# Optimization experiments

Measured on AMD Instinct MI355X. Metric: run time of the kernel, lower is better.

Reference implementation:

```python
import jax, jax.numpy as jnp
import numpy as np

LABEL_SIZE = 64
START = LABEL_SIZE - 2
STOP = LABEL_SIZE - 1
NEG = -10000.0


def setup_inputs() -> dict:
    key = jax.random.key(0)
    k1, k2 = jax.random.split(key)
    B, T, L = 512, 512, LABEL_SIZE
    emissions = jax.random.normal(k1, (B, T, L), dtype=jnp.float32)
    # xavier-uniform-ish init, then mask row START (nothing transitions INTO start
    # ... actually transitions[next, prev]: row START = transitions into START)
    bound = float(np.sqrt(6.0 / (L + L)))
    trans = jax.random.uniform(k2, (L, L), dtype=jnp.float32, minval=-bound, maxval=bound)
    trans = trans.at[START, :].set(NEG)   # never transition to START
    trans = trans.at[:, STOP].set(NEG)    # never transition from STOP
    return {"input": emissions, "transitions": trans}


def reference(input, transitions):
    # input: [B, T, L] emission scores; transitions[next_tag, prev_tag]: [L, L]
    B, T, L = input.shape
    init = jnp.full((B, L), NEG, dtype=input.dtype).at[:, START].set(0.0)

    def step(forward_var, emit_t):
        # forward_var: [B, L] (over prev tag); emit_t: [B, L] (over next tag)
        # scores[b, next, prev] = forward_var[b, prev] + transitions[next, prev]
        nv = jax.nn.logsumexp(forward_var[:, None, :] + transitions[None, :, :], axis=-1)
        return nv + emit_t, None

    forward_var, _ = jax.lax.scan(step, init, jnp.swapaxes(input, 0, 1))  # scan over T
    terminal = forward_var + transitions[STOP][None, :]
    return jax.nn.logsumexp(terminal, axis=-1)  # [B] log partition function
```

## Files before the change

### kernel.cpp

```cpp
#include <hip/hip_runtime.h>

#define NTAG 64
#define TLEN 512
#define START_TAG 62
#define STOP_TAG 63
#define NB 16

typedef __attribute__((ext_vector_type(4))) float    f32x4;
typedef __attribute__((ext_vector_type(8))) short    s16x8;
typedef __attribute__((ext_vector_type(2))) unsigned u32x2;
typedef __attribute__((ext_vector_type(4))) unsigned u32x4;

#if __has_builtin(__builtin_amdgcn_exp2f)
#define EXP2(x) __builtin_amdgcn_exp2f(x)
#else
#define EXP2(x) exp2f(x)
#endif

__device__ __forceinline__ unsigned cvtpk_bf16(float lo, float hi) {
    unsigned r;
    asm("v_cvt_pk_bf16_f32 %0, %1, %2" : "=v"(r) : "v"(lo), "v"(hi));
    return r;
}

__device__ __forceinline__ f32x4 mfma32(s16x8 a, s16x8 b, f32x4 c) {
    return __builtin_amdgcn_mfma_f32_16x16x32_bf16(a, b, c, 0, 0, 0);
}

__global__ __launch_bounds__(128) void crf_fwd_bwd(
    const float* __restrict__ emis,
    const float* __restrict__ trans,
    float* __restrict__ out)
{
    const int tile = blockIdx.x;
    const int tid  = threadIdx.x;
    const int lane = tid & 63;
    const int w    = tid >> 6;
    const int c    = lane & 15;
    const int g    = lane >> 4;
    const int b0   = tile * NB;

    const float L2E = 1.4426950408889634f;
    const float LN2 = 0.6931471805599453f;

    __shared__ float fy[64][17];
    __shared__ int   offb_sh[16];

    s16x8 Af[4][2];
    #pragma unroll
    for (int m = 0; m < 4; ++m) {
        #pragma unroll
        for (int kt = 0; kt < 2; ++kt) {
            float ev[8];
            #pragma unroll
            for (int jj = 0; jj < 8; ++jj) {
                const int r = 16 * m + c;
                const int k = 32 * kt + 16 * (jj >> 2) + 4 * g + (jj & 3);
                const float tv = (w == 0) ? trans[r * NTAG + k]
                                          : trans[k * NTAG + r];
                ev[jj] = EXP2(tv * L2E);
            }
            u32x4 p;
            p[0] = cvtpk_bf16(ev[0], ev[1]);
            p[1] = cvtpk_bf16(ev[2], ev[3]);
            p[2] = cvtpk_bf16(ev[4], ev[5]);
            p[3] = cvtpk_bf16(ev[6], ev[7]);
            Af[m][kt] = __builtin_bit_cast(s16x8, p);
        }
    }

    const float* ebase = emis + (size_t)(b0 + c) * (TLEN * NTAG) + 4 * g;

    f32x4 wq[8][4];
    f32x4 peA[4], peB[4];
    u32x2 Bf[4];
    f32x4 ym[4];
    int   off = 0;
    int   erA = 0, erB = 0;

    #define PREF_F(slot, t) do {                                       \
        const float* _p = ebase + (t) * NTAG;                          \
        wq[slot][0] = *(const f32x4*)(_p +  0);                        \
        wq[slot][1] = *(const f32x4*)(_p + 16);                        \
        wq[slot][2] = *(const f32x4*)(_p + 32);                        \
        wq[slot][3] = *(const f32x4*)(_p + 48);                        \
    } while (0)
    #define PREF_B(slot, tp) PREF_F(slot, 510 - (tp))

    #define EXPQ(dst, slot) do {                                       \
        _Pragma("unroll")                                              \
        for (int m_ = 0; m_ < 4; ++m_) {                               \
            dst[m_][0] = EXP2(wq[slot][m_][0] * L2E);                  \
            dst[m_][1] = EXP2(wq[slot][m_][1] * L2E);                  \
            dst[m_][2] = EXP2(wq[slot][m_][2] * L2E);                  \
            dst[m_][3] = EXP2(wq[slot][m_][3] * L2E);                  \
        }                                                              \
    } while (0)

    #define BCAT(i) __builtin_bit_cast(s16x8,                          \
        (u32x4){Bf[2*(i)].x, Bf[2*(i)].y, Bf[2*(i)+1].x, Bf[2*(i)+1].y})

    #define MFMA_ALL() do {                                            \
        s16x8 B0_ = BCAT(0), B1_ = BCAT(1);                            \
        f32x4 a0 = {0.f,0.f,0.f,0.f}, a1 = a0, a2 = a0, a3 = a0;       \
        a0 = mfma32(Af[0][0], B0_, a0); a1 = mfma32(Af[1][0], B0_, a1);\
        a2 = mfma32(Af[2][0], B0_, a2); a3 = mfma32(Af[3][0], B0_, a3);\
        a0 = mfma32(Af[0][1], B1_, a0); a1 = mfma32(Af[1][1], B1_, a1);\
        a2 = mfma32(Af[2][1], B1_, a2); a3 = mfma32(Af[3][1], B1_, a3);\
        ym[0] = a0; ym[1] = a1; ym[2] = a2; ym[3] = a3;                \
    } while (0)

    #define PACK() do {                                                \
        Bf[0].x = cvtpk_bf16(ym[0][0], ym[0][1]);                      \
        Bf[0].y = cvtpk_bf16(ym[0][2], ym[0][3]);                      \
        Bf[1].x = cvtpk_bf16(ym[1][0], ym[1][1]);                      \
        Bf[1].y = cvtpk_bf16(ym[1][2], ym[1][3]);                      \
        Bf[2].x = cvtpk_bf16(ym[2][0], ym[2][1]);                      \
        Bf[2].y = cvtpk_bf16(ym[2][2], ym[2][3]);                      \
        Bf[3].x = cvtpk_bf16(ym[3][0], ym[3][1]);                      \
        Bf[3].y = cvtpk_bf16(ym[3][2], ym[3][3]);                      \
    } while (0)

    #define COLMAX_TO(dst, mxv) do {                                   \
        float _m = (mxv);                                              \
        const float _s1 = __shfl_xor(_m, 16, 64);                      \
        const float _s2 = __shfl_xor(_m, 32, 64);                      \
        const float _s3 = __shfl_xor(_m, 48, 64);                      \
        _m = fmaxf(fmaxf(_m, _s1), fmaxf(_s2, _s3));                   \
        const int _ef = (int)((__float_as_uint(_m) >> 23) & 0xffu);    \
        dst = (_ef == 0 || _ef == 0xff) ? 0 : _ef - 127;               \
    } while (0)

    #define CSTEP_E(u, PEC, PEN, ERAPP, ERMEAS, PRFM, tb) do {         \
        off += ERAPP;                                                  \
        const float rs_ =                                              \
            __uint_as_float((unsigned)(127 - (ERAPP)) << 23);          \
        MFMA_ALL();                                                    \
        EXPQ(PEN, ((u) + 1) & 7);                                     \
        ym[0] = ym[0] * PEC[0] * rs_; ym[1] = ym[1] * PEC[1] * rs_;    \
        ym[2] = ym[2] * PEC[2] * rs_; ym[3] = ym[3] * PEC[3] * rs_;    \
        PACK();                                                        \
        float mx_ = fmaxf(fmaxf(fmaxf(ym[0][0], ym[0][1]),             \
                                fmaxf(ym[0][2], ym[0][3])),            \
                          fmaxf(fmaxf(ym[1][0], ym[1][1]),             \
                                fmaxf(ym[1][2], ym[1][3])));           \
        mx_ = fmaxf(mx_, fmaxf(fmaxf(ym[2][0], ym[2][1]),              \
                               fmaxf(ym[2][2], ym[2][3])));            \
        mx_ = fmaxf(mx_, fmaxf(fmaxf(ym[3][0], ym[3][1]),              \
                               fmaxf(ym[3][2], ym[3][3])));            \
        COLMAX_TO(ERMEAS, mx_);                                        \
        PRFM((u), (tb) + (u) + 8);                                     \
    } while (0)

    #define CSTEP_O(u, PEC, PEN, PRFM, tb) do {                        \
        MFMA_ALL();                                                    \
        EXPQ(PEN, ((u) + 1) & 7);                                     \
        ym[0] *= PEC[0]; ym[1] *= PEC[1];                              \
        ym[2] *= PEC[2]; ym[3] *= PEC[3];                              \
        PACK();                                                        \
        PRFM((u), (tb) + (u) + 8);                                     \
    } while (0)

    #define OCTET(PRFM, tb)                                            \
        CSTEP_E(0, peA, peB, erB, erA, PRFM, tb);                      \
        CSTEP_O(1, peB, peA, PRFM, tb);                                \
        CSTEP_E(2, peA, peB, erA, erB, PRFM, tb);                      \
        CSTEP_O(3, peB, peA, PRFM, tb);                                \
        CSTEP_E(4, peA, peB, erB, erA, PRFM, tb);                      \
        CSTEP_O(5, peB, peA, PRFM, tb);                                \
        CSTEP_E(6, peA, peB, erA, erB, PRFM, tb);                      \
        CSTEP_O(7, peB, peA, PRFM, tb);

    if (w == 0) {
        Bf[0].x = 0u; Bf[0].y = 0u; Bf[1] = Bf[0]; Bf[2] = Bf[0];
        Bf[3].x = 0u; Bf[3].y = (g == 3) ? 0x3f80u : 0u;
        erA = 0; erB = 0;

        PREF_F(0, 0); PREF_F(1, 1); PREF_F(2, 2); PREF_F(3, 3);
        PREF_F(4, 4); PREF_F(5, 5); PREF_F(6, 6); PREF_F(7, 7);
        EXPQ(peA, 0);

        #pragma clang loop unroll(disable)
        for (int it = 0; it < 32; ++it) {
            const int tb = it * 8;
            OCTET(PREF_F, tb)
        }
    } else {
        float smx = 0.f;
        #pragma unroll
        for (int m = 0; m < 4; ++m) {
            f32x4 wv = *(const f32x4*)(ebase + 511 * NTAG + 16 * m);
            float v[4];
            #pragma unroll
            for (int j = 0; j < 4; ++j) {
                const int r = 16 * m + 4 * g + j;
                v[j] = EXP2((trans[STOP_TAG * NTAG + r] + wv[j]) * L2E);
                smx = fmaxf(smx, v[j]);
            }
            Bf[m].x = cvtpk_bf16(v[0], v[1]);
            Bf[m].y = cvtpk_bf16(v[2], v[3]);
        }
        COLMAX_TO(erB, smx);
        erA = 0;

        PREF_B(0, 0); PREF_B(1, 1); PREF_B(2, 2); PREF_B(3, 3);
        PREF_B(4, 4); PREF_B(5, 5); PREF_B(6, 6); PREF_B(7, 7);
        EXPQ(peA, 0);

        #pragma clang loop unroll(disable)
        for (int it = 0; it < 31; ++it) {
            const int tb = it * 8;
            OCTET(PREF_B, tb)
        }
        {
            const int tb = 248;
            CSTEP_E(0, peA, peB, erB, erA, PREF_B, tb);
            CSTEP_O(1, peB, peA, PREF_B, tb);
            CSTEP_E(2, peA, peB, erA, erB, PREF_B, tb);
            CSTEP_O(3, peB, peA, PREF_B, tb);
            CSTEP_E(4, peA, peB, erB, erA, PREF_B, tb);
            CSTEP_O(5, peB, peA, PREF_B, tb);
            CSTEP_E(6, peA, peB, erA, erB, PREF_B, tb);
        }
        off += erB;
        const float rs = __uint_as_float((unsigned)(127 - erB) << 23);
        MFMA_ALL();
        ym[0] *= rs; ym[1] *= rs; ym[2] *= rs; ym[3] *= rs;

        #pragma unroll
        for (int m = 0; m < 4; ++m)
            #pragma unroll
            for (int j = 0; j < 4; ++j)
                fy[lane][4 * m + j] = ym[m][j];
        if (lane < 16) offb_sh[lane] = off;
    }

    __syncthreads();

    if (w == 0) {
        float p = 0.f;
        #pragma unroll
        for (int m = 0; m < 4; ++m)
            #pragma unroll
            for (int j = 0; j < 4; ++j)
                p = fmaf(ym[m][j], fy[lane][4 * m + j], p);
        p += __shfl_xor(p, 16, 64);
        p += __shfl_xor(p, 32, 64);
        if (lane < 16)
            out[b0 + lane] = LN2 * (log2f(p) + (float)(off + offb_sh[lane]));
    }

    #undef PREF_F
    #undef PREF_B
    #undef EXPQ
    #undef BCAT
    #undef MFMA_ALL
    #undef PACK
    #undef COLMAX_TO
    #undef CSTEP_E
    #undef CSTEP_O
    #undef OCTET
}

extern "C" void kernel_launch(void* const* d_in, const int* in_sizes, int n_in,
                              void* d_out, int out_size, void* d_ws, size_t ws_size,
                              hipStream_t stream) {
    const float* emis  = (const float*)d_in[0];
    const float* trans = (const float*)d_in[1];
    float* out = (float*)d_out;
    (void)in_sizes; (void)n_in; (void)out_size; (void)d_ws; (void)ws_size;
    crf_fwd_bwd<<<512 / NB, 128, 0, stream>>>(emis, trans, out);
}
```

Measured before the change: 159.7 us.

## Precompute exponentiated bf16 emissions in a parallel prepass before the serial recurrence

Adds a grid-wide prepass kernel that computes exp(emissions) and stores it as bf16 in the workspace. The recurrence kernel then loads half-width precomputed values and unpacks them with shifts instead of doing per-step exp2 on its critical path. The rescale factor is folded into the emission unpack on odd steps rather than applied on even steps. This costs an extra kernel launch and a full extra pass of emission traffic, and it falls back to the old kernel when the workspace is too small.

```diff
diff --git a/kernel.cpp b/kernel.cpp
--- a/kernel.cpp
+++ b/kernel.cpp
@@ -5,6 +5,8 @@
 #define START_TAG 62
 #define STOP_TAG 63
 #define NB 16
+#define PE_ELEMS ((size_t)512 * 512 * 64)
+#define PE_BYTES (PE_ELEMS * 2)
 
 typedef __attribute__((ext_vector_type(4))) float    f32x4;
 typedef __attribute__((ext_vector_type(8))) short    s16x8;
@@ -27,8 +29,74 @@
     return __builtin_amdgcn_mfma_f32_16x16x32_bf16(a, b, c, 0, 0, 0);
 }
 
+__global__ __launch_bounds__(256) void pe_prepass(
+    const float* __restrict__ emis, unsigned short* __restrict__ pe)
+{
+    const float L2E = 1.4426950408889634f;
+    const size_t n8 = PE_ELEMS / 8;
+    for (size_t i = (size_t)blockIdx.x * 256 + threadIdx.x; i < n8;
+         i += (size_t)gridDim.x * 256) {
+        f32x4 a = ((const f32x4*)emis)[2 * i];
+        f32x4 b = ((const f32x4*)emis)[2 * i + 1];
+        u32x4 o;
+        o[0] = cvtpk_bf16(EXP2(a[0] * L2E), EXP2(a[1] * L2E));
+        o[1] = cvtpk_bf16(EXP2(a[2] * L2E), EXP2(a[3] * L2E));
+        o[2] = cvtpk_bf16(EXP2(b[0] * L2E), EXP2(b[1] * L2E));
+        o[3] = cvtpk_bf16(EXP2(b[2] * L2E), EXP2(b[3] * L2E));
+        ((u32x4*)pe)[i] = o;
+    }
+}
+
+#define RSOF(e) __uint_as_float((unsigned)(127 - (e)) << 23)
+
+#define BCAT(i) __builtin_bit_cast(s16x8,                          \
+    (u32x4){Bf[2*(i)].x, Bf[2*(i)].y, Bf[2*(i)+1].x, Bf[2*(i)+1].y})
+
+#define MFMA_ALL() do {                                            \
+    s16x8 B0_ = BCAT(0), B1_ = BCAT(1);                            \
+    f32x4 a0 = {0.f,0.f,0.f,0.f}, a1 = a0, a2 = a0, a3 = a0;       \
+    a0 = mfma32(Af[0][0], B0_, a0); a1 = mfma32(Af[1][0], B0_, a1);\
+    a2 = mfma32(Af[2][0], B0_, a2); a3 = mfma32(Af[3][0], B0_, a3);\
+    a0 = mfma32(Af[0][1], B1_, a0); a1 = mfma32(Af[1][1], B1_, a1);\
+    a2 = mfma32(Af[2][1], B1_, a2); a3 = mfma32(Af[3][1], B1_, a3);\
+    ym[0] = a0; ym[1] = a1; ym[2] = a2; ym[3] = a3;                \
+} while (0)
+
+#define PACK() do {                                                \
+    Bf[0].x = cvtpk_bf16(ym[0][0], ym[0][1]);                      \
+    Bf[0].y = cvtpk_bf16(ym[0][2], ym[0][3]);                      \
+    Bf[1].x = cvtpk_bf16(ym[1][0], ym[1][1]);                      \
+    Bf[1].y = cvtpk_bf16(ym[1][2], ym[1][3]);                      \
+    Bf[2].x = cvtpk_bf16(ym[2][0], ym[2][1]);                      \
+    Bf[2].y = cvtpk_bf16(ym[2][2], ym[2][3]);                      \
+    Bf[3].x = cvtpk_bf16(ym[3][0], ym[3][1]);                      \
+    Bf[3].y = cvtpk_bf16(ym[3][2], ym[3][3]);                      \
+} while (0)
+
+#define COLMAX_TO(dst, mxv) do {                                   \
+    float _m = (mxv);                                              \
+    const float _s1 = __shfl_xor(_m, 16, 64);                      \
+    const float _s2 = __shfl_xor(_m, 32, 64);                      \
+    const float _s3 = __shfl_xor(_m, 48, 64);                      \
+    _m = fmaxf(fmaxf(_m, _s1), fmaxf(_s2, _s3));                   \
+    const int _ef = (int)((__float_as_uint(_m) >> 23) & 0xffu);    \
+    dst = (_ef == 0 || _ef == 0xff) ? 0 : _ef - 127;               \
+} while (0)
+
+#define YMAX(mxv) do {                                             \
+    mxv = fmaxf(fmaxf(fmaxf(ym[0][0], ym[0][1]),                   \
+                      fmaxf(ym[0][2], ym[0][3])),                  \
+                fmaxf(fmaxf(ym[1][0], ym[1][1]),                   \
+                      fmaxf(ym[1][2], ym[1][3])));                 \
+    mxv = fmaxf(mxv, fmaxf(fmaxf(ym[2][0], ym[2][1]),              \
+                           fmaxf(ym[2][2], ym[2][3])));            \
+    mxv = fmaxf(mxv, fmaxf(fmaxf(ym[3][0], ym[3][1]),              \
+                           fmaxf(ym[3][2], ym[3][3])));            \
+} while (0)
+
 __global__ __launch_bounds__(128) void crf_fwd_bwd(
     const float* __restrict__ emis,
+    const unsigned short* __restrict__ pe,
     const float* __restrict__ trans,
     float* __restrict__ out)
 {
@@ -70,6 +138,211 @@
     }
 
     const float* ebase = emis + (size_t)(b0 + c) * (TLEN * NTAG) + 4 * g;
+    const unsigned short* pebase = pe + (size_t)(b0 + c) * (TLEN * NTAG) + 4 * g;
+
+    u32x2 wq[8][4];
+    f32x4 peA[4], peB[4];
+    u32x2 Bf[4];
+    f32x4 ym[4];
+    int   off = 0;
+    int   erA = 0, erB = 0;
+
+    #define PREF_F(slot, t) do {                                       \
+        const unsigned short* _p = pebase + (size_t)(t) * NTAG;        \
+        wq[slot][0] = *(const u32x2*)(_p +  0);                        \
+        wq[slot][1] = *(const u32x2*)(_p + 16);                        \
+        wq[slot][2] = *(const u32x2*)(_p + 32);                        \
+        wq[slot][3] = *(const u32x2*)(_p + 48);                        \
+    } while (0)
+    #define PREF_B(slot, tp) PREF_F(slot, 510 - (tp))
+
+    #define PEPREP_N(dst, slot) do {                                   \
+        _Pragma("unroll")                                              \
+        for (int m_ = 0; m_ < 4; ++m_) {                               \
+            const unsigned _w0 = wq[slot][m_].x;                       \
+            const unsigned _w1 = wq[slot][m_].y;                       \
+            dst[m_][0] = __uint_as_float(_w0 << 16);                   \
+            dst[m_][1] = __uint_as_float(_w0 & 0xffff0000u);           \
+            dst[m_][2] = __uint_as_float(_w1 << 16);                   \
+            dst[m_][3] = __uint_as_float(_w1 & 0xffff0000u);           \
+        }                                                              \
+    } while (0)
+    #define PEPREP_S(dst, slot, ev) do {                               \
+        const float _rsp = RSOF(ev);                                   \
+        _Pragma("unroll")                                              \
+        for (int m_ = 0; m_ < 4; ++m_) {                               \
+            const unsigned _w0 = wq[slot][m_].x;                       \
+            const unsigned _w1 = wq[slot][m_].y;                       \
+            dst[m_][0] = __uint_as_float(_w0 << 16) * _rsp;            \
+            dst[m_][1] = __uint_as_float(_w0 & 0xffff0000u) * _rsp;    \
+            dst[m_][2] = __uint_as_float(_w1 << 16) * _rsp;            \
+            dst[m_][3] = __uint_as_float(_w1 & 0xffff0000u) * _rsp;    \
+        }                                                              \
+    } while (0)
+
+    #define CSTEP_E(u, PEC, PEN, ERAPP, ERMEAS, PRFM, tb) do {         \
+        off += ERAPP;                                                  \
+        MFMA_ALL();                                                    \
+        PEPREP_N(PEN, ((u) + 1) & 7);                                  \
+        ym[0] *= PEC[0]; ym[1] *= PEC[1];                              \
+        ym[2] *= PEC[2]; ym[3] *= PEC[3];                              \
+        PACK();                                                        \
+        float mx_;                                                     \
+        YMAX(mx_);                                                     \
+        COLMAX_TO(ERMEAS, mx_);                                        \
+        PRFM((u), (tb) + (u) + 8);                                     \
+    } while (0)
+
+    #define CSTEP_O(u, PEC, PEN, ERNX, PRFM, tb) do {                  \
+        MFMA_ALL();                                                    \
+        PEPREP_S(PEN, ((u) + 1) & 7, ERNX);                            \
+        ym[0] *= PEC[0]; ym[1] *= PEC[1];                              \
+        ym[2] *= PEC[2]; ym[3] *= PEC[3];                              \
+        PACK();                                                        \
+        PRFM((u), (tb) + (u) + 8);                                     \
+    } while (0)
+
+    #define OCTET(PRFM, tb)                                            \
+        CSTEP_E(0, peA, peB, erB, erA, PRFM, tb);                      \
+        CSTEP_O(1, peB, peA, erA, PRFM, tb);                           \
+        CSTEP_E(2, peA, peB, erA, erB, PRFM, tb);                      \
+        CSTEP_O(3, peB, peA, erB, PRFM, tb);                           \
+        CSTEP_E(4, peA, peB, erB, erA, PRFM, tb);                      \
+        CSTEP_O(5, peB, peA, erA, PRFM, tb);                           \
+        CSTEP_E(6, peA, peB, erA, erB, PRFM, tb);                      \
+        CSTEP_O(7, peB, peA, erB, PRFM, tb);
+
+    if (w == 0) {
+        Bf[0].x = 0u; Bf[0].y = 0u; Bf[1] = Bf[0]; Bf[2] = Bf[0];
+        Bf[3].x = 0u; Bf[3].y = (g == 3) ? 0x3f80u : 0u;
+        erA = 0; erB = 0;
+
+        PREF_F(0, 0); PREF_F(1, 1); PREF_F(2, 2); PREF_F(3, 3);
+        PREF_F(4, 4); PREF_F(5, 5); PREF_F(6, 6); PREF_F(7, 7);
+        PEPREP_S(peA, 0, erB);
+
+        #pragma clang loop unroll(disable)
+        for (int it = 0; it < 32; ++it) {
+            const int tb = it * 8;
+            OCTET(PREF_F, tb)
+        }
+    } else {
+        float smx = 0.f;
+        #pragma unroll
+        for (int m = 0; m < 4; ++m) {
+            f32x4 wv = *(const f32x4*)(ebase + 511 * NTAG + 16 * m);
+            float v[4];
+            #pragma unroll
+            for (int j = 0; j < 4; ++j) {
+                const int r = 16 * m + 4 * g + j;
+                v[j] = EXP2((trans[STOP_TAG * NTAG + r] + wv[j]) * L2E);
+                smx = fmaxf(smx, v[j]);
+            }
+            Bf[m].x = cvtpk_bf16(v[0], v[1]);
+            Bf[m].y = cvtpk_bf16(v[2], v[3]);
+        }
+        COLMAX_TO(erB, smx);
+        erA = 0;
+
+        PREF_B(0, 0); PREF_B(1, 1); PREF_B(2, 2); PREF_B(3, 3);
+        PREF_B(4, 4); PREF_B(5, 5); PREF_B(6, 6); PREF_B(7, 7);
+        PEPREP_S(peA, 0, erB);
+
+        #pragma clang loop unroll(disable)
+        for (int it = 0; it < 31; ++it) {
+            const int tb = it * 8;
+            OCTET(PREF_B, tb)
+        }
+        {
+            const int tb = 248;
+            CSTEP_E(0, peA, peB, erB, erA, PREF_B, tb);
+            CSTEP_O(1, peB, peA, erA, PREF_B, tb);
+            CSTEP_E(2, peA, peB, erA, erB, PREF_B, tb);
+            CSTEP_O(3, peB, peA, erB, PREF_B, tb);
+            CSTEP_E(4, peA, peB, erB, erA, PREF_B, tb);
+            CSTEP_O(5, peB, peA, erA, PREF_B, tb);
+            CSTEP_E(6, peA, peB, erA, erB, PREF_B, tb);
+        }
+        off += erB;
+        const float rs = RSOF(erB);
+        MFMA_ALL();
+        ym[0] *= rs; ym[1] *= rs; ym[2] *= rs; ym[3] *= rs;
+
+        #pragma unroll
+        for (int m = 0; m < 4; ++m)
+            #pragma unroll
+            for (int j = 0; j < 4; ++j)
+                fy[lane][4 * m + j] = ym[m][j];
+        if (lane < 16) offb_sh[lane] = off;
+    }
+
+    __syncthreads();
+
+    if (w == 0) {
+        float p = 0.f;
+        #pragma unroll
+        for (int m = 0; m < 4; ++m)
+            #pragma unroll
+            for (int j = 0; j < 4; ++j)
+                p = fmaf(ym[m][j], fy[lane][4 * m + j], p);
+        p += __shfl_xor(p, 16, 64);
+        p += __shfl_xor(p, 32, 64);
+        if (lane < 16)
+            out[b0 + lane] = LN2 * (log2f(p) + (float)(off + offb_sh[lane]));
+    }
+
+    #undef PREF_F
+    #undef PREF_B
+    #undef PEPREP_N
+    #undef PEPREP_S
+    #undef CSTEP_E
+    #undef CSTEP_O
+    #undef OCTET
+}
+
+__global__ __launch_bounds__(128) void crf_fwd_bwd_fb(
+    const float* __restrict__ emis,
+    const float* __restrict__ trans,
+    float* __restrict__ out)
+{
+    const int tile = blockIdx.x;
+    const int tid  = threadIdx.x;
+    const int lane = tid & 63;
+    const int w    = tid >> 6;
+    const int c    = lane & 15;
+    const int g    = lane >> 4;
+    const int b0   = tile * NB;
+
+    const float L2E = 1.4426950408889634f;
+    const float LN2 = 0.6931471805599453f;
+
+    __shared__ float fy[64][17];
+    __shared__ int   offb_sh[16];
+
+    s16x8 Af[4][2];
+    #pragma unroll
+    for (int m = 0; m < 4; ++m) {
+        #pragma unroll
+        for (int kt = 0; kt < 2; ++kt) {
+            float ev[8];
+            #pragma unroll
+            for (int jj = 0; jj < 8; ++jj) {
+                const int r = 16 * m + c;
+                const int k = 32 * kt + 16 * (jj >> 2) + 4 * g + (jj & 3);
+                const float tv = (w == 0) ? trans[r * NTAG + k]
+                                          : trans[k * NTAG + r];
+                ev[jj] = EXP2(tv * L2E);
+            }
+            u32x4 p;
+            p[0] = cvtpk_bf16(ev[0], ev[1]);
+            p[1] = cvtpk_bf16(ev[2], ev[3]);
+            p[2] = cvtpk_bf16(ev[4], ev[5]);
+            p[3] = cvtpk_bf16(ev[6], ev[7]);
+            Af[m][kt] = __builtin_bit_cast(s16x8, p);
+        }
+    }
+
+    const float* ebase = emis + (size_t)(b0 + c) * (TLEN * NTAG) + 4 * g;
 
     f32x4 wq[8][4];
     f32x4 peA[4], peB[4];
@@ -78,16 +351,16 @@
     int   off = 0;
     int   erA = 0, erB = 0;
 
-    #define PREF_F(slot, t) do {                                       \
+    #define PREF_FE(slot, t) do {                                      \
         const float* _p = ebase + (t) * NTAG;                          \
         wq[slot][0] = *(const f32x4*)(_p +  0);                        \
         wq[slot][1] = *(const f32x4*)(_p + 16);                        \
         wq[slot][2] = *(const f32x4*)(_p + 32);                        \
         wq[slot][3] = *(const f32x4*)(_p + 48);                        \
     } while (0)
-    #define PREF_B(slot, tp) PREF_F(slot, 510 - (tp))
-
-    #define EXPQ(dst, slot) do {                                       \
+    #define PREF_BE(slot, tp) PREF_FE(slot, 510 - (tp))
+
+    #define FEXPQ(dst, slot) do {                                      \
         _Pragma("unroll")                                              \
         for (int m_ = 0; m_ < 4; ++m_) {                               \
             dst[m_][0] = EXP2(wq[slot][m_][0] * L2E);                  \
@@ -97,93 +370,52 @@
         }                                                              \
     } while (0)
 
-    #define BCAT(i) __builtin_bit_cast(s16x8,                          \
-        (u32x4){Bf[2*(i)].x, Bf[2*(i)].y, Bf[2*(i)+1].x, Bf[2*(i)+1].y})
-
-    #define MFMA_ALL() do {                                            \
-        s16x8 B0_ = BCAT(0), B1_ = BCAT(1);                            \
-        f32x4 a0 = {0.f,0.f,0.f,0.f}, a1 = a0, a2 = a0, a3 = a0;       \
-        a0 = mfma32(Af[0][0], B0_, a0); a1 = mfma32(Af[1][0], B0_, a1);\
-        a2 = mfma32(Af[2][0], B0_, a2); a3 = mfma32(Af[3][0], B0_, a3);\
-        a0 = mfma32(Af[0][1], B1_, a0); a1 = mfma32(Af[1][1], B1_, a1);\
-        a2 = mfma32(Af[2][1], B1_, a2); a3 = mfma32(Af[3][1], B1_, a3);\
-        ym[0] = a0; ym[1] = a1; ym[2] = a2; ym[3] = a3;                \
-    } while (0)
-
-    #define PACK() do {                                                \
-        Bf[0].x = cvtpk_bf16(ym[0][0], ym[0][1]);                      \
-        Bf[0].y = cvtpk_bf16(ym[0][2], ym[0][3]);                      \
-        Bf[1].x = cvtpk_bf16(ym[1][0], ym[1][1]);                      \
-        Bf[1].y = cvtpk_bf16(ym[1][2], ym[1][3]);                      \
-        Bf[2].x = cvtpk_bf16(ym[2][0], ym[2][1]);                      \
-        Bf[2].y = cvtpk_bf16(ym[2][2], ym[2][3]);                      \
-        Bf[3].x = cvtpk_bf16(ym[3][0], ym[3][1]);                      \
-        Bf[3].y = cvtpk_bf16(ym[3][2], ym[3][3]);                      \
-    } while (0)
-
-    #define COLMAX_TO(dst, mxv) do {                                   \
-        float _m = (mxv);                                              \
-        const float _s1 = __shfl_xor(_m, 16, 64);                      \
-        const float _s2 = __shfl_xor(_m, 32, 64);                      \
-        const float _s3 = __shfl_xor(_m, 48, 64);                      \
-        _m = fmaxf(fmaxf(_m, _s1), fmaxf(_s2, _s3));                   \
-        const int _ef = (int)((__float_as_uint(_m) >> 23) & 0xffu);    \
-        dst = (_ef == 0 || _ef == 0xff) ? 0 : _ef - 127;               \
-    } while (0)
-
-    #define CSTEP_E(u, PEC, PEN, ERAPP, ERMEAS, PRFM, tb) do {         \
+    #define FCSTEP_E(u, PEC, PEN, ERAPP, ERMEAS, PRFM, tb) do {        \
         off += ERAPP;                                                  \
-        const float rs_ =                                              \
-            __uint_as_float((unsigned)(127 - (ERAPP)) << 23);          \
+        const float rs_ = RSOF(ERAPP);                                 \
         MFMA_ALL();                                                    \
-        EXPQ(PEN, ((u) + 1) & 7);                                     \
+        FEXPQ(PEN, ((u) + 1) & 7);                                     \
         ym[0] = ym[0] * PEC[0] * rs_; ym[1] = ym[1] * PEC[1] * rs_;    \
         ym[2] = ym[2] * PEC[2] * rs_; ym[3] = ym[3] * PEC[3] * rs_;    \
         PACK();                                                        \
-        float mx_ = fmaxf(fmaxf(fmaxf(ym[0][0], ym[0][1]),             \
-                                fmaxf(ym[0][2], ym[0][3])),            \
-                          fmaxf(fmaxf(ym[1][0], ym[1][1]),             \
-                                fmaxf(ym[1][2], ym[1][3])));           \
-        mx_ = fmaxf(mx_, fmaxf(fmaxf(ym[2][0], ym[2][1]),              \
-                               fmaxf(ym[2][2], ym[2][3])));            \
-        mx_ = fmaxf(mx_, fmaxf(fmaxf(ym[3][0], ym[3][1]),              \
-                               fmaxf(ym[3][2], ym[3][3])));            \
+        float mx_;                                                     \
+        YMAX(mx_);                                                     \
         COLMAX_TO(ERMEAS, mx_);                                        \
         PRFM((u), (tb) + (u) + 8);                                     \
     } while (0)
 
-    #define CSTEP_O(u, PEC, PEN, PRFM, tb) do {                        \
+    #define FCSTEP_O(u, PEC, PEN, PRFM, tb) do {                       \
         MFMA_ALL();                                                    \
-        EXPQ(PEN, ((u) + 1) & 7);                                     \
+        FEXPQ(PEN, ((u) + 1) & 7);                                     \
         ym[0] *= PEC[0]; ym[1] *= PEC[1];                              \
         ym[2] *= PEC[2]; ym[3] *= PEC[3];                              \
         PACK();                                                        \
         PRFM((u), (tb) + (u) + 8);                                     \
     } while (0)
 
-    #define OCTET(PRFM, tb)                                            \
-        CSTEP_E(0, peA, peB, erB, erA, PRFM, tb);                      \
-        CSTEP_O(1, peB, peA, PRFM, tb);                                \
-        CSTEP_E(2, peA, peB, erA, erB, PRFM, tb);                      \
-        CSTEP_O(3, peB, peA, PRFM, tb);                                \
-        CSTEP_E(4, peA, peB, erB, erA, PRFM, tb);                      \
-        CSTEP_O(5, peB, peA, PRFM, tb);                                \
-        CSTEP_E(6, peA, peB, erA, erB, PRFM, tb);                      \
-        CSTEP_O(7, peB, peA, PRFM, tb);
+    #define FOCTET(PRFM, tb)                                           \
+        FCSTEP_E(0, peA, peB, erB, erA, PRFM, tb);                     \
+        FCSTEP_O(1, peB, peA, PRFM, tb);                               \
+        FCSTEP_E(2, peA, peB, erA, erB, PRFM, tb);                     \
+        FCSTEP_O(3, peB, peA, PRFM, tb);                               \
+        FCSTEP_E(4, peA, peB, erB, erA, PRFM, tb);                     \
+        FCSTEP_O(5, peB, peA, PRFM, tb);                               \
+        FCSTEP_E(6, peA, peB, erA, erB, PRFM, tb);                     \
+        FCSTEP_O(7, peB, peA, PRFM, tb);
 
     if (w == 0) {
         Bf[0].x = 0u; Bf[0].y = 0u; Bf[1] = Bf[0]; Bf[2] = Bf[0];
         Bf[3].x = 0u; Bf[3].y = (g == 3) ? 0x3f80u : 0u;
         erA = 0; erB = 0;
 
-        PREF_F(0, 0); PREF_F(1, 1); PREF_F(2, 2); PREF_F(3, 3);
-        PREF_F(4, 4); PREF_F(5, 5); PREF_F(6, 6); PREF_F(7, 7);
-        EXPQ(peA, 0);
+        PREF_FE(0, 0); PREF_FE(1, 1); PREF_FE(2, 2); PREF_FE(3, 3);
+        PREF_FE(4, 4); PREF_FE(5, 5); PREF_FE(6, 6); PREF_FE(7, 7);
+        FEXPQ(peA, 0);
 
         #pragma clang loop unroll(disable)
         for (int it = 0; it < 32; ++it) {
             const int tb = it * 8;
-            OCTET(PREF_F, tb)
+            FOCTET(PREF_FE, tb)
         }
     } else {
         float smx = 0.f;
@@ -203,27 +435,27 @@
         COLMAX_TO(erB, smx);
         erA = 0;
 
-        PREF_B(0, 0); PREF_B(1, 1); PREF_B(2, 2); PREF_B(3, 3);
-        PREF_B(4, 4); PREF_B(5, 5); PREF_B(6, 6); PREF_B(7, 7);
-        EXPQ(peA, 0);
+        PREF_BE(0, 0); PREF_BE(1, 1); PREF_BE(2, 2); PREF_BE(3, 3);
+        PREF_BE(4, 4); PREF_BE(5, 5); PREF_BE(6, 6); PREF_BE(7, 7);
+        FEXPQ(peA, 0);
 
         #pragma clang loop unroll(disable)
         for (int it = 0; it < 31; ++it) {
             const int tb = it * 8;
-            OCTET(PREF_B, tb)
+            FOCTET(PREF_BE, tb)
         }
         {
             const int tb = 248;
-            CSTEP_E(0, peA, peB, erB, erA, PREF_B, tb);
-            CSTEP_O(1, peB, peA, PREF_B, tb);
-            CSTEP_E(2, peA, peB, erA, erB, PREF_B, tb);
-            CSTEP_O(3, peB, peA, PREF_B, tb);
-            CSTEP_E(4, peA, peB, erB, erA, PREF_B, tb);
-            CSTEP_O(5, peB, peA, PREF_B, tb);
-            CSTEP_E(6, peA, peB, erA, erB, PREF_B, tb);
+            FCSTEP_E(0, peA, peB, erB, erA, PREF_BE, tb);
+            FCSTEP_O(1, peB, peA, PREF_BE, tb);
+            FCSTEP_E(2, peA, peB, erA, erB, PREF_BE, tb);
+            FCSTEP_O(3, peB, peA, PREF_BE, tb);
+            FCSTEP_E(4, peA, peB, erB, erA, PREF_BE, tb);
+            FCSTEP_O(5, peB, peA, PREF_BE, tb);
+            FCSTEP_E(6, peA, peB, erA, erB, PREF_BE, tb);
         }
         off += erB;
-        const float rs = __uint_as_float((unsigned)(127 - erB) << 23);
+        const float rs = RSOF(erB);
         MFMA_ALL();
         ym[0] *= rs; ym[1] *= rs; ym[2] *= rs; ym[3] *= rs;
 
@@ -250,16 +482,12 @@
             out[b0 + lane] = LN2 * (log2f(p) + (float)(off + offb_sh[lane]));
     }
 
-    #undef PREF_F
-    #undef PREF_B
-    #undef EXPQ
-    #undef BCAT
-    #undef MFMA_ALL
-    #undef PACK
-    #undef COLMAX_TO
-    #undef CSTEP_E
-    #undef CSTEP_O
-    #undef OCTET
+    #undef PREF_FE
+    #undef PREF_BE
+    #undef FEXPQ
+    #undef FCSTEP_E
+    #undef FCSTEP_O
+    #undef FOCTET
 }
 
 extern "C" void kernel_launch(void* const* d_in, const int* in_sizes, int n_in,
@@ -268,6 +496,12 @@
     const float* emis  = (const float*)d_in[0];
     const float* trans = (const float*)d_in[1];
     float* out = (float*)d_out;
-    (void)in_sizes; (void)n_in; (void)out_size; (void)d_ws; (void)ws_size;
-    crf_fwd_bwd<<<512 / NB, 128, 0, stream>>>(emis, trans, out);
+    (void)in_sizes; (void)n_in; (void)out_size;
+    if (d_ws != nullptr && ws_size >= PE_BYTES) {
+        unsigned short* pe = (unsigned short*)d_ws;
+        pe_prepass<<<2048, 256, 0, stream>>>(emis, pe);
+        crf_fwd_bwd<<<512 / NB, 128, 0, stream>>>(emis, pe, trans, out);
+    } else {
+        crf_fwd_bwd_fb<<<512 / NB, 128, 0, stream>>>(emis, trans, out);
+    }
 }
```

Measured after the change: 181.6 us. 13.7% more time.
